# Optimization experiments

Hardware: AMD Instinct MI355X
Metric: run time of the kernel (lower is better)

Reference implementation:

```python
import jax, jax.numpy as jnp
from jax import lax
import numpy as np

H = 200           # mpnn_hidden_size
DEPTH = 3         # mpnn_depth
ATOM_FDIM = 39
BOND_FDIM = 11
B, NA, NB = 128, 48, 96   # molecules, atoms/mol, bonds/mol (padded fixed size)
L, VOCAB = 1000, 26       # protein length, amino-acid vocab
KERNALS = [3, 5, 7]
PROT_FILTERS = [50, 96, 128, 200]
FC_DIMS = [400, 200, 100, 1]


def setup_inputs() -> dict:
    key = jax.random.key(0)
    ks = jax.random.split(key, 32)
    s = 0.05
    inp = {}
    inp["fatoms"] = jax.random.normal(ks[0], (B, NA, ATOM_FDIM), jnp.float32)
    inp["fbonds"] = jax.random.normal(ks[1], (B, NB, ATOM_FDIM + BOND_FDIM), jnp.float32)
    inp["agraph"] = jax.random.randint(ks[2], (B, NA, 6), 0, NB)
    inp["bgraph"] = jax.random.randint(ks[3], (B, NB, 6), 0, NB)
    inp["protein_seq"] = jax.random.randint(ks[4], (B, L), 0, VOCAB)
    # MPNN weights (stored as (in, out) matrices; W_i and W_h have no bias)
    inp["W_i"] = jax.random.normal(ks[5], (ATOM_FDIM + BOND_FDIM, H), jnp.float32) * s
    inp["W_h"] = jax.random.normal(ks[6], (H, H), jnp.float32) * s
    inp["W_o_w"] = jax.random.normal(ks[7], (ATOM_FDIM + H, H), jnp.float32) * s
    inp["W_o_b"] = jax.random.normal(ks[8], (H,), jnp.float32) * s
    # protein embedding + CNN
    inp["embed_protein"] = jax.random.normal(ks[9], (VOCAB, PROT_FILTERS[0]), jnp.float32) * s
    for i, k in enumerate(KERNALS):
        inp[f"conv{i}_w"] = jax.random.normal(ks[10 + 2 * i], (PROT_FILTERS[i + 1], PROT_FILTERS[i], k), jnp.float32) * s
        inp[f"conv{i}_b"] = jax.random.normal(ks[11 + 2 * i], (PROT_FILTERS[i + 1],), jnp.float32) * s
    # CPI fc head 400 -> 200 -> 100 -> 1
    for i in range(3):
        inp[f"fc{i}_w"] = jax.random.normal(ks[16 + 2 * i], (FC_DIMS[i], FC_DIMS[i + 1]), jnp.float32) * s
        inp[f"fc{i}_b"] = jax.random.normal(ks[17 + 2 * i], (FC_DIMS[i + 1],), jnp.float32) * s
    return inp


def reference(fatoms, fbonds, agraph, bgraph, protein_seq,
              W_i, W_h, W_o_w, W_o_b, embed_protein,
              conv0_w, conv0_b, conv1_w, conv1_b, conv2_w, conv2_b,
              fc0_w, fc0_b, fc1_w, fc1_b, fc2_w, fc2_b):
    # ---- MPNN over all molecules (vmapped single_molecule_forward) ----
    def mol(fa, fb, ag, bg):
        binput = fb @ W_i                      # (NB, H)
        message = jax.nn.relu(binput)
        for _ in range(DEPTH - 1):
            nei = message[bg].sum(axis=1)      # gather (NB,6,H) -> sum -> (NB,H)
            message = jax.nn.relu(binput + nei @ W_h)
        nei = message[ag].sum(axis=1)          # (NA, H)
        atom_h = jax.nn.relu(jnp.concatenate([fa, nei], axis=1) @ W_o_w + W_o_b)
        return atom_h.mean(axis=0)             # (H,)

    embeddings = jax.vmap(mol)(fatoms, fbonds, agraph, bgraph)  # (B, H)

    # ---- protein CNN tower ----
    pv = embed_protein[protein_seq]            # (B, L, 50)
    pv = pv.transpose(0, 2, 1)                 # (B, 50, L)
    for w, b, k in ((conv0_w, conv0_b, KERNALS[0]),
                    (conv1_w, conv1_b, KERNALS[1]),
                    (conv2_w, conv2_b, KERNALS[2])):
        pv = lax.conv_general_dilated(pv, w, window_strides=(1,),
                                      padding=[(k // 2, k // 2)],
                                      dimension_numbers=("NCH", "OIH", "NCH"))
        pv = jax.nn.relu(pv + b[None, :, None])
    protein_vector = pv.max(axis=2)            # adaptive_max_pool1d(out=1) -> (B, 200)

    # ---- CPI fc head ----
    x = jnp.concatenate([embeddings, protein_vector], axis=1)  # (B, 400)
    x = jax.nn.relu(x @ fc0_w + fc0_b)
    x = jax.nn.relu(x @ fc1_w + fc1_b)
    x = x @ fc2_w + fc2_b
    return x                                   # (B, 1)
```

## Files before the change

kernel.cpp:

```cpp
#include <hip/hip_runtime.h>
#include <hip/hip_bf16.h>
#include <cstddef>

#define H 200
#define NA 48
#define NBB 96
#define BATCH 128
#define AFD 39
#define BFD 50
#define LP 1000
#define CATD (AFD + H)
#define APB 8
#define BIPB 16

typedef unsigned short ushort_t;
typedef __bf16 bf16x8 __attribute__((ext_vector_type(8)));
typedef float f32x16 __attribute__((ext_vector_type(16)));
typedef unsigned uint32x4 __attribute__((ext_vector_type(4)));

union U16B { uint4 u; bf16x8 b; };
static __device__ __forceinline__ bf16x8 as_bf16x8(uint4 u) { U16B x; x.u = u; return x.b; }
union U16B2 { uint32x4 u; bf16x8 b; };
static __device__ __forceinline__ bf16x8 as_bf16x8v(uint32x4 u) { U16B2 x; x.u = u; return x.b; }

static __device__ __forceinline__ ushort_t f2bf(float f) {
    union { float f; unsigned u; } a; a.f = f;
    unsigned r = (a.u + 0x7FFFu + ((a.u >> 16) & 1u)) >> 16;
    return (ushort_t)r;
}

static __device__ __forceinline__ uint32x4 gload16(const ushort_t* base, unsigned voff) {
    uint32x4 r;
    asm volatile("global_load_dwordx4 %0, %1, %2"
                 : "=&v"(r) : "v"(voff), "s"(base));
    return r;
}

template <int COUT, int CIN, int CP, int K>
static __device__ __forceinline__ void prep_one(int t, const float* __restrict__ w,
                                                ushort_t* __restrict__ Wb) {
    constexpr int NC = CP / 16;
    constexpr int NS = K * NC;
    int j = t & 7;
    int lane = (t >> 3) & 63;
    int s = (t >> 9) % NS;
    int ct = (t >> 9) / NS;
    int co = ct * 32 + (lane & 31);
    int tt = s / NC, cc = s % NC;
    int ci = cc * 16 + ((lane >> 5) & 1) * 8 + j;
    float v = 0.f;
    if (co < COUT && ci < CIN) v = w[((size_t)co * CIN + ci) * K + tt];
    Wb[t] = f2bf(v);
}

#define MNS 13
#define PREP_T0 (4 * 12 * 512)
#define PREP_T1 (PREP_T0 + 4 * 30 * 512)
#define PREP_T2 (PREP_T1 + 8 * 56 * 512)
#define PREP_T3 (PREP_T2 + 51200)
#define PREP_T4 (PREP_T3 + 8 * MNS * 512)

__global__ __launch_bounds__(256) void k_prep_all(
        const float* __restrict__ c0w, const float* __restrict__ c1w,
        const float* __restrict__ c2w, const float* __restrict__ Wh,
        float* __restrict__ x,
        ushort_t* __restrict__ Wb0, ushort_t* __restrict__ Wb1,
        ushort_t* __restrict__ Wb2, ushort_t* __restrict__ Wbh) {
    int tid = blockIdx.x * 256 + threadIdx.x;
    if (tid < PREP_T0) prep_one<96, 50, 64, 3>(tid, c0w, Wb0);
    else if (tid < PREP_T1) prep_one<128, 96, 96, 5>(tid - PREP_T0, c1w, Wb1);
    else if (tid < PREP_T2) prep_one<200, 128, 128, 7>(tid - PREP_T1, c2w, Wb2);
    else if (tid < PREP_T3) x[tid - PREP_T2] = 0.f;
    else if (tid < PREP_T4) {
        int t = tid - PREP_T3;
        int j = t & 7;
        int lane = (t >> 3) & 63;
        int s = (t >> 9) % MNS;
        int tile = (t >> 9) / MNS;
        int co = tile * 32 + (lane & 31);
        int ci = s * 16 + ((lane >> 5) & 1) * 8 + j;
        float v = 0.f;
        if (co < H && ci < H) v = Wh[ci * H + co];
        Wbh[t] = f2bf(v);
    }
}

template <int CP, int K, int COUT, int CO_WAVES, int L_WAVES, bool FMAX, bool EMB>
static __device__ __forceinline__ void conv_body(
        const ushort_t* __restrict__ act, const int* __restrict__ seq,
        const float* __restrict__ emb, const ushort_t* __restrict__ Wb,
        const float* __restrict__ bias, void* __restrict__ outv,
        ushort_t* __restrict__ Xs) {
    constexpr int NC = CP / 16;
    constexpr int NS = K * NC;
    constexpr int P = K / 2;
    constexpr int PITCH = CP + 8;
    constexpr int LTILE = 64 * L_WAVES;
    constexpr int ROWS = LTILE + K - 1;
    constexpr int CPR = CP / 8;
    constexpr int D = 4;

    int b = blockIdx.z, lb = blockIdx.x;
    int l0 = lb * LTILE;
    int tid = threadIdx.x;

    if (EMB) {
        const int* seqb = seq + (size_t)b * LP;
        for (int idx = tid; idx < ROWS * CPR; idx += 256) {
            int r = idx / CPR, c = idx % CPR;
            int l = l0 - P + r;
            uint4 v = {0u, 0u, 0u, 0u};
            if ((unsigned)l < (unsigned)LP) {
                int s = seqb[l];
                const float* e = emb + (size_t)s * 50;
                ushort_t h[8];
#pragma unroll
                for (int j = 0; j < 8; ++j) {
                    int cc = c * 8 + j;
                    h[j] = (cc < 50) ? f2bf(e[cc]) : (ushort_t)0;
                }
                v.x = (unsigned)h[0] | ((unsigned)h[1] << 16);
                v.y = (unsigned)h[2] | ((unsigned)h[3] << 16);
                v.z = (unsigned)h[4] | ((unsigned)h[5] << 16);
                v.w = (unsigned)h[6] | ((unsigned)h[7] << 16);
            }
            *(uint4*)(Xs + r * PITCH + c * 8) = v;
        }
    } else {
        const ushort_t* actb = act + (size_t)b * LP * CP;
        for (int idx = tid; idx < ROWS * CPR; idx += 256) {
            int r = idx / CPR, c = idx % CPR;
            int l = l0 - P + r;
            uint4 v = {0u, 0u, 0u, 0u};
            if ((unsigned)l < (unsigned)LP) v = *(const uint4*)(actb + (size_t)l * CP + c * 8);
            *(uint4*)(Xs + r * PITCH + c * 8) = v;
        }
    }

    int lane = tid & 63, wv = tid >> 6;
    int cw = wv % CO_WAVES, lw = wv / CO_WAVES;
    int ln31 = lane & 31, half = lane >> 5;

    unsigned abase0 = (unsigned)(cw * 2) * (unsigned)NS * 1024u + (unsigned)lane * 16u;
    unsigned abase1 = abase0 + (unsigned)NS * 1024u;
    int bbase = (lw * 64 + ln31) * PITCH + half * 8;

    f32x16 acc[2][2];
#pragma unroll
    for (int ct = 0; ct < 2; ++ct)
#pragma unroll
        for (int lt = 0; lt < 2; ++lt)
#pragma unroll
            for (int r = 0; r < 16; ++r) acc[ct][lt][r] = 0.f;

    __syncthreads();

    uint32x4 ra0[D], ra1[D];
#pragma unroll
    for (int d = 0; d < D; ++d) {
        ra0[d] = gload16(Wb, abase0 + (unsigned)(d * 1024));
        ra1[d] = gload16(Wb, abase1 + (unsigned)(d * 1024));
    }

    uint4 bC0 = *(const uint4*)(Xs + bbase);
    uint4 bC1 = *(const uint4*)(Xs + bbase + 32 * PITCH);

#pragma unroll
    for (int s = 0; s < NS; ++s) {
        int sn = (s + 1 < NS) ? s + 1 : NS - 1;
        int tn = sn / NC, ccn = sn % NC;
        int off = bbase + tn * PITCH + ccn * 16;
        uint4 bN0 = *(const uint4*)(Xs + off);
        uint4 bN1 = *(const uint4*)(Xs + off + 32 * PITCH);

        {
            const int rem = NS - 1 - s;
            const int allow = 2 * ((D - 1) < rem ? (D - 1) : rem);
            asm volatile("s_waitcnt vmcnt(%0)" :: "i"(allow) : "memory");
            __builtin_amdgcn_sched_barrier(0);
        }

        uint32x4 a0 = ra0[s % D];
        uint32x4 a1 = ra1[s % D];

        acc[0][0] = __builtin_amdgcn_mfma_f32_32x32x16_bf16(
            as_bf16x8v(a0), as_bf16x8(bC0), acc[0][0], 0, 0, 0);
        acc[1][0] = __builtin_amdgcn_mfma_f32_32x32x16_bf16(
            as_bf16x8v(a1), as_bf16x8(bC0), acc[1][0], 0, 0, 0);
        acc[0][1] = __builtin_amdgcn_mfma_f32_32x32x16_bf16(
            as_bf16x8v(a0), as_bf16x8(bC1), acc[0][1], 0, 0, 0);
        acc[1][1] = __builtin_amdgcn_mfma_f32_32x32x16_bf16(
            as_bf16x8v(a1), as_bf16x8(bC1), acc[1][1], 0, 0, 0);

        if (s + D < NS) {
            ra0[s % D] = gload16(Wb, abase0 + (unsigned)((s + D) * 1024));
            ra1[s % D] = gload16(Wb, abase1 + (unsigned)((s + D) * 1024));
        }

        bC0 = bN0; bC1 = bN1;
    }

    if (!FMAX) {
        ushort_t* out = (ushort_t*)outv + (size_t)b * LP * COUT;
#pragma unroll
        for (int ct = 0; ct < 2; ++ct) {
            int cbase = (cw * 2 + ct) * 32 + 4 * half;
#pragma unroll
            for (int g = 0; g < 4; ++g) {
                int co = cbase + 8 * g;
                if (co >= COUT) continue;
                float4 bv = *(const float4*)(bias + co);
#pragma unroll
                for (int lt = 0; lt < 2; ++lt) {
                    int l = l0 + lw * 64 + lt * 32 + ln31;
                    if (l < LP) {
                        ushort_t h0 = f2bf(fmaxf(acc[ct][lt][4 * g + 0] + bv.x, 0.f));
                        ushort_t h1 = f2bf(fmaxf(acc[ct][lt][4 * g + 1] + bv.y, 0.f));
                        ushort_t h2 = f2bf(fmaxf(acc[ct][lt][4 * g + 2] + bv.z, 0.f));
                        ushort_t h3 = f2bf(fmaxf(acc[ct][lt][4 * g + 3] + bv.w, 0.f));
                        uint2 o;
                        o.x = (unsigned)h0 | ((unsigned)h1 << 16);
                        o.y = (unsigned)h2 | ((unsigned)h3 << 16);
                        *(uint2*)(out + (size_t)l * COUT + co) = o;
                    }
                }
            }
        }
    } else {
        float* xout = (float*)outv;
#pragma unroll
        for (int ct = 0; ct < 2; ++ct) {
            float mx[16];
#pragma unroll
            for (int r = 0; r < 16; ++r) mx[r] = -3.0e38f;
#pragma unroll
            for (int lt = 0; lt < 2; ++lt) {
                int l = l0 + lw * 64 + lt * 32 + ln31;
                if (l < LP) {
#pragma unroll
                    for (int r = 0; r < 16; ++r) mx[r] = fmaxf(mx[r], acc[ct][lt][r]);
                }
            }
#pragma unroll
            for (int r = 0; r < 16; ++r) {
#pragma unroll
                for (int off = 1; off < 32; off <<= 1)
                    mx[r] = fmaxf(mx[r], __shfl_xor(mx[r], off, 64));
            }
            if (ln31 == 0) {
                int cbase = (cw * 2 + ct) * 32 + 4 * half;
#pragma unroll
                for (int r = 0; r < 16; ++r) {
                    int co = cbase + (r & 3) + 8 * (r >> 2);
                    if (co < COUT) {
                        float v = fmaxf(mx[r] + bias[co], 0.f);
                        atomicMax((int*)&xout[(size_t)b * 400 + 200 + co], __float_as_int(v));
                    }
                }
            }
        }
    }
}

__global__ __launch_bounds__(256, 3) void k_conv0(
        const int* __restrict__ seq, const float* __restrict__ emb,
        const ushort_t* __restrict__ Wb, const float* __restrict__ bias,
        ushort_t* __restrict__ out) {
    __shared__ __align__(16) ushort_t Xs[(128 + 2) * (64 + 8)];
    conv_body<64, 3, 96, 2, 2, false, true>(nullptr, seq, emb, Wb, bias, out, Xs);
}
__global__ __launch_bounds__(256, 3) void k_conv1(
        const ushort_t* __restrict__ act, const ushort_t* __restrict__ Wb,
        const float* __restrict__ bias, ushort_t* __restrict__ out) {
    __shared__ __align__(16) ushort_t Xs[(128 + 4) * (96 + 8)];
    conv_body<96, 5, 128, 2, 2, false, false>(act, nullptr, nullptr, Wb, bias, out, Xs);
}
__global__ __launch_bounds__(256, 3) void k_conv2(
        const ushort_t* __restrict__ act, const ushort_t* __restrict__ Wb,
        const float* __restrict__ bias, float* __restrict__ x) {
    __shared__ __align__(16) ushort_t Xs[(64 + 6) * (128 + 8)];
    conv_body<128, 7, 200, 4, 1, true, false>(act, nullptr, nullptr, Wb, bias, x, Xs);
}

__global__ __launch_bounds__(256) void k_bond_input(
        const float* __restrict__ fbonds, const float* __restrict__ Wi,
        float* __restrict__ binput, float* __restrict__ msg) {
    int bond0 = blockIdx.x * BIPB;
    __shared__ float fb[BIPB][BFD];
    int tid = threadIdx.x;
    for (int idx = tid; idx < BIPB * BFD; idx += 256)
        fb[idx / BFD][idx % BFD] = fbonds[(size_t)bond0 * BFD + idx];
    __syncthreads();
    if (tid < H) {
        float acc[BIPB];
#pragma unroll
        for (int q = 0; q < BIPB; ++q) acc[q] = 0.f;
#pragma unroll 5
        for (int k = 0; k < BFD; ++k) {
            float w = Wi[k * H + tid];
#pragma unroll
            for (int q = 0; q < BIPB; ++q) acc[q] += fb[q][k] * w;
        }
#pragma unroll
        for (int q = 0; q < BIPB; ++q) {
            size_t o = (size_t)(bond0 + q) * H + tid;
            binput[o] = acc[q];
            msg[o] = fmaxf(acc[q], 0.f);
        }
    }
}

#define MPITCH 216
__global__ __launch_bounds__(256) void k_msg_mfma(
        const float* __restrict__ msgIn, const float* __restrict__ binput,
        const int* __restrict__ bgraph, const ushort_t* __restrict__ Wbh,
        float* __restrict__ msgOut) {
    __shared__ __align__(16) ushort_t Xs[32 * MPITCH];
    __shared__ int idxs[32 * 6];
    constexpr int D = 4;
    int m0 = blockIdx.x * 32;
    int tid = threadIdx.x;

    if (tid < 192) {
        int r = tid / 6, j = tid - r * 6;
        int m = m0 + r;
        int mol = m / NBB;
        idxs[tid] = mol * NBB + bgraph[(size_t)m * 6 + j];
    }
    __syncthreads();

    for (int it = tid; it < 32 * 26; it += 256) {
        int r = it / 26, c = it - r * 26;
        uint4 v = {0u, 0u, 0u, 0u};
        if (c < 25) {
            float sv[8];
#pragma unroll
            for (int k = 0; k < 8; ++k) sv[k] = 0.f;
#pragma unroll
            for (int j = 0; j < 6; ++j) {
                const float* row = msgIn + (size_t)idxs[r * 6 + j] * H + c * 8;
                float4 a = *(const float4*)row;
                float4 b = *(const float4*)(row + 4);
                sv[0] += a.x; sv[1] += a.y; sv[2] += a.z; sv[3] += a.w;
                sv[4] += b.x; sv[5] += b.y; sv[6] += b.z; sv[7] += b.w;
            }
            v.x = (unsigned)f2bf(sv[0]) | ((unsigned)f2bf(sv[1]) << 16);
            v.y = (unsigned)f2bf(sv[2]) | ((unsigned)f2bf(sv[3]) << 16);
            v.z = (unsigned)f2bf(sv[4]) | ((unsigned)f2bf(sv[5]) << 16);
            v.w = (unsigned)f2bf(sv[6]) | ((unsigned)f2bf(sv[7]) << 16);
        }
        *(uint4*)(Xs + r * MPITCH + c * 8) = v;
    }

    int lane = tid & 63, wv = tid >> 6;
    int ln31 = lane & 31, half = lane >> 5;
    unsigned abase0 = (unsigned)(wv * 2) * (unsigned)MNS * 1024u + (unsigned)lane * 16u;
    unsigned abase1 = abase0 + (unsigned)MNS * 1024u;
    int bbase = ln31 * MPITCH + half * 8;

    f32x16 acc[2];
#pragma unroll
    for (int ct = 0; ct < 2; ++ct)
#pragma unroll
        for (int r = 0; r < 16; ++r) acc[ct][r] = 0.f;

    __syncthreads();

    uint32x4 ra0[D], ra1[D];
#pragma unroll
    for (int d = 0; d < D; ++d) {
        ra0[d] = gload16(Wbh, abase0 + (unsigned)(d * 1024));
        ra1[d] = gload16(Wbh, abase1 + (unsigned)(d * 1024));
    }

    uint4 bC = *(const uint4*)(Xs + bbase);

#pragma unroll
    for (int s = 0; s < MNS; ++s) {
        int sn = (s + 1 < MNS) ? s + 1 : MNS - 1;
        uint4 bN = *(const uint4*)(Xs + bbase + sn * 16);

        {
            const int rem = MNS - 1 - s;
            const int allow = 2 * ((D - 1) < rem ? (D - 1) : rem);
            asm volatile("s_waitcnt vmcnt(%0)" :: "i"(allow) : "memory");
            __builtin_amdgcn_sched_barrier(0);
        }

        uint32x4 a0 = ra0[s % D];
        uint32x4 a1 = ra1[s % D];
        acc[0] = __builtin_amdgcn_mfma_f32_32x32x16_bf16(
            as_bf16x8v(a0), as_bf16x8(bC), acc[0], 0, 0, 0);
        acc[1] = __builtin_amdgcn_mfma_f32_32x32x16_bf16(
            as_bf16x8v(a1), as_bf16x8(bC), acc[1], 0, 0, 0);

        if (s + D < MNS) {
            ra0[s % D] = gload16(Wbh, abase0 + (unsigned)((s + D) * 1024));
            ra1[s % D] = gload16(Wbh, abase1 + (unsigned)((s + D) * 1024));
        }
        bC = bN;
    }

    int m = m0 + ln31;
    const float* bi = binput + (size_t)m * H;
    float* outp = msgOut + (size_t)m * H;
#pragma unroll
    for (int ct = 0; ct < 2; ++ct) {
        int cbase = (wv * 2 + ct) * 32 + 4 * half;
#pragma unroll
        for (int g = 0; g < 4; ++g) {
            int co = cbase + 8 * g;
            if (co >= H) continue;
            float4 b4 = *(const float4*)(bi + co);
            float4 o;
            o.x = fmaxf(acc[ct][4 * g + 0] + b4.x, 0.f);
            o.y = fmaxf(acc[ct][4 * g + 1] + b4.y, 0.f);
            o.z = fmaxf(acc[ct][4 * g + 2] + b4.z, 0.f);
            o.w = fmaxf(acc[ct][4 * g + 3] + b4.w, 0.f);
            *(float4*)(outp + co) = o;
        }
    }
}

__global__ __launch_bounds__(256) void k_atom(
        const float* __restrict__ msg, const float* __restrict__ fatoms,
        const int* __restrict__ agraph, const float* __restrict__ Wo,
        const float* __restrict__ Wob, float* __restrict__ x) {
    const int grpPerMol = NA / APB;
    int b = blockIdx.x / grpPerMol;
    int grp = blockIdx.x % grpPerMol;
    int atom0 = grp * APB;
    __shared__ int idxs[APB * 6];
    __shared__ float cat[APB][CATD];
    int tid = threadIdx.x;
    if (tid < APB * 6) idxs[tid] = agraph[((size_t)(b * NA + atom0)) * 6 + tid];
    for (int idx = tid; idx < APB * AFD; idx += 256) {
        int q = idx / AFD, c = idx % AFD;
        cat[q][c] = fatoms[((size_t)(b * NA + atom0 + q)) * AFD + c];
    }
    __syncthreads();
    if (tid < H) {
        const float* base = msg + (size_t)b * NBB * H;
#pragma unroll
        for (int q = 0; q < APB; ++q) {
            float s = 0.f;
#pragma unroll
            for (int j = 0; j < 6; ++j) s += base[(size_t)idxs[q * 6 + j] * H + tid];
            cat[q][AFD + tid] = s;
        }
    }
    __syncthreads();
    if (tid < H) {
        float bb = Wob[tid];
        float acc[APB];
#pragma unroll
        for (int q = 0; q < APB; ++q) acc[q] = bb;
#pragma unroll 4
        for (int k = 0; k < CATD; ++k) {
            float w = Wo[k * H + tid];
#pragma unroll
            for (int q = 0; q < APB; ++q) acc[q] += cat[q][k] * w;
        }
        float s = 0.f;
#pragma unroll
        for (int q = 0; q < APB; ++q) s += fmaxf(acc[q], 0.f);
        atomicAdd(&x[(size_t)b * 400 + tid], s * (1.f / NA));
    }
}

__global__ __launch_bounds__(256) void k_fc(
        const float* __restrict__ x,
        const float* __restrict__ w0, const float* __restrict__ b0,
        const float* __restrict__ w1, const float* __restrict__ b1,
        const float* __restrict__ w2, const float* __restrict__ b2,
        float* __restrict__ out) {
    int b = blockIdx.x, tid = threadIdx.x;
    __shared__ float xr[400];
    __shared__ float h1[200];
    __shared__ float h2[100];
    for (int i = tid; i < 400; i += 256) xr[i] = x[(size_t)b * 400 + i];
    __syncthreads();
    if (tid < 200) {
        float a = b0[tid];
#pragma unroll 4
        for (int k = 0; k < 400; ++k) a += xr[k] * w0[k * 200 + tid];
        h1[tid] = fmaxf(a, 0.f);
    }
    __syncthreads();
    if (tid < 100) {
        float a = b1[tid];
#pragma unroll 4
        for (int k = 0; k < 200; ++k) a += h1[k] * w1[k * 100 + tid];
        h2[tid] = fmaxf(a, 0.f);
    }
    __syncthreads();
    if (tid == 0) {
        float a = b2[0];
#pragma unroll 4
        for (int k = 0; k < 100; ++k) a += h2[k] * w2[k];
        out[b] = a;
    }
}

extern "C" void kernel_launch(void* const* d_in, const int* in_sizes, int n_in,
                              void* d_out, int out_size, void* d_ws, size_t ws_size,
                              hipStream_t stream) {
    const float* fatoms = (const float*)d_in[0];
    const float* fbonds = (const float*)d_in[1];
    const int* agraph = (const int*)d_in[2];
    const int* bgraph = (const int*)d_in[3];
    const int* seq = (const int*)d_in[4];
    const float* Wi = (const float*)d_in[5];
    const float* Wh = (const float*)d_in[6];
    const float* Wo = (const float*)d_in[7];
    const float* Wob = (const float*)d_in[8];
    const float* embp = (const float*)d_in[9];
    const float* c0w = (const float*)d_in[10];
    const float* c0b = (const float*)d_in[11];
    const float* c1w = (const float*)d_in[12];
    const float* c1b = (const float*)d_in[13];
    const float* c2w = (const float*)d_in[14];
    const float* c2b = (const float*)d_in[15];
    const float* fc0w = (const float*)d_in[16];
    const float* fc0b = (const float*)d_in[17];
    const float* fc1w = (const float*)d_in[18];
    const float* fc1b = (const float*)d_in[19];
    const float* fc2w = (const float*)d_in[20];
    const float* fc2b = (const float*)d_in[21];

    float* ws = (float*)d_ws;
    float* binput = ws;
    float* msgA = binput + 2457600;
    float* msgB = msgA + 2457600;
    float* x = msgB + 2457600;
    ushort_t* u = (ushort_t*)(x + 51200);
    ushort_t* act1 = u;
    ushort_t* act2 = act1 + 12288000;
    ushort_t* Wb0 = act2 + 16384000;
    ushort_t* Wb1 = Wb0 + 24576;
    ushort_t* Wb2 = Wb1 + 61440;
    ushort_t* Wbh = Wb2 + 229376;

    k_prep_all<<<(PREP_T4 + 255) / 256, 256, 0, stream>>>(c0w, c1w, c2w, Wh, x,
                                                          Wb0, Wb1, Wb2, Wbh);

    k_bond_input<<<BATCH * NBB / BIPB, 256, 0, stream>>>(fbonds, Wi, binput, msgA);
    k_msg_mfma<<<BATCH * NBB / 32, 256, 0, stream>>>(msgA, binput, bgraph, Wbh, msgB);
    k_msg_mfma<<<BATCH * NBB / 32, 256, 0, stream>>>(msgB, binput, bgraph, Wbh, msgA);
    k_atom<<<BATCH * NA / APB, 256, 0, stream>>>(msgA, fatoms, agraph, Wo, Wob, x);

    k_conv0<<<dim3(8, 1, BATCH), 256, 0, stream>>>(seq, embp, Wb0, c0b, act1);
    k_conv1<<<dim3(8, 1, BATCH), 256, 0, stream>>>(act1, Wb1, c1b, act2);
    k_conv2<<<dim3(16, 1, BATCH), 256, 0, stream>>>(act2, Wb2, c2b, x);

    k_fc<<<BATCH, 256, 0, stream>>>(x, fc0w, fc0b, fc1w, fc1b, fc2w, fc2b, (float*)d_out);
}
```

Baseline: 345.2 us.

## Horizontally fuse independent MPNN and protein CNN kernels into shared launches

Merges the weight-prep and bond-input kernels into one launch. It also pairs each message-passing step, and then the atom readout, with a conv layer of the protein tower in a single grid, dispatching on blockIdx.x, so that 9 launches become 5. The MPNN and CNN branches are independent, so their blocks can run concurrently and fill the GPU better while paying fewer launch gaps. The cost is that shared-memory buffers are aliased between the branches and that the message kernel now inherits the conv kernels' (256,3) launch bounds. That can tighten its register budget and cause spills.

After: 331.0 us. -4.1%, faster.

```diff
diff --git a/kernel.cpp b/kernel.cpp
--- a/kernel.cpp
+++ b/kernel.cpp
@@ -59,14 +59,14 @@
 #define PREP_T2 (PREP_T1 + 8 * 56 * 512)
 #define PREP_T3 (PREP_T2 + 51200)
 #define PREP_T4 (PREP_T3 + 8 * MNS * 512)
-
-__global__ __launch_bounds__(256) void k_prep_all(
-        const float* __restrict__ c0w, const float* __restrict__ c1w,
+#define PREP_BLKS (PREP_T4 / 256)
+
+static __device__ __forceinline__ void prep_body(
+        int tid, const float* __restrict__ c0w, const float* __restrict__ c1w,
         const float* __restrict__ c2w, const float* __restrict__ Wh,
-        float* __restrict__ x,
-        ushort_t* __restrict__ Wb0, ushort_t* __restrict__ Wb1,
-        ushort_t* __restrict__ Wb2, ushort_t* __restrict__ Wbh) {
-    int tid = blockIdx.x * 256 + threadIdx.x;
+        float* __restrict__ x, ushort_t* __restrict__ Wb0,
+        ushort_t* __restrict__ Wb1, ushort_t* __restrict__ Wb2,
+        ushort_t* __restrict__ Wbh) {
     if (tid < PREP_T0) prep_one<96, 50, 64, 3>(tid, c0w, Wb0);
     else if (tid < PREP_T1) prep_one<128, 96, 96, 5>(tid - PREP_T0, c1w, Wb1);
     else if (tid < PREP_T2) prep_one<200, 128, 128, 7>(tid - PREP_T1, c2w, Wb2);
@@ -262,63 +262,13 @@
     }
 }
 
-__global__ __launch_bounds__(256, 3) void k_conv0(
-        const int* __restrict__ seq, const float* __restrict__ emb,
-        const ushort_t* __restrict__ Wb, const float* __restrict__ bias,
-        ushort_t* __restrict__ out) {
-    __shared__ __align__(16) ushort_t Xs[(128 + 2) * (64 + 8)];
-    conv_body<64, 3, 96, 2, 2, false, true>(nullptr, seq, emb, Wb, bias, out, Xs);
-}
-__global__ __launch_bounds__(256, 3) void k_conv1(
-        const ushort_t* __restrict__ act, const ushort_t* __restrict__ Wb,
-        const float* __restrict__ bias, ushort_t* __restrict__ out) {
-    __shared__ __align__(16) ushort_t Xs[(128 + 4) * (96 + 8)];
-    conv_body<96, 5, 128, 2, 2, false, false>(act, nullptr, nullptr, Wb, bias, out, Xs);
-}
-__global__ __launch_bounds__(256, 3) void k_conv2(
-        const ushort_t* __restrict__ act, const ushort_t* __restrict__ Wb,
-        const float* __restrict__ bias, float* __restrict__ x) {
-    __shared__ __align__(16) ushort_t Xs[(64 + 6) * (128 + 8)];
-    conv_body<128, 7, 200, 4, 1, true, false>(act, nullptr, nullptr, Wb, bias, x, Xs);
-}
-
-__global__ __launch_bounds__(256) void k_bond_input(
-        const float* __restrict__ fbonds, const float* __restrict__ Wi,
-        float* __restrict__ binput, float* __restrict__ msg) {
-    int bond0 = blockIdx.x * BIPB;
-    __shared__ float fb[BIPB][BFD];
-    int tid = threadIdx.x;
-    for (int idx = tid; idx < BIPB * BFD; idx += 256)
-        fb[idx / BFD][idx % BFD] = fbonds[(size_t)bond0 * BFD + idx];
-    __syncthreads();
-    if (tid < H) {
-        float acc[BIPB];
-#pragma unroll
-        for (int q = 0; q < BIPB; ++q) acc[q] = 0.f;
-#pragma unroll 5
-        for (int k = 0; k < BFD; ++k) {
-            float w = Wi[k * H + tid];
-#pragma unroll
-            for (int q = 0; q < BIPB; ++q) acc[q] += fb[q][k] * w;
-        }
-#pragma unroll
-        for (int q = 0; q < BIPB; ++q) {
-            size_t o = (size_t)(bond0 + q) * H + tid;
-            binput[o] = acc[q];
-            msg[o] = fmaxf(acc[q], 0.f);
-        }
-    }
-}
-
 #define MPITCH 216
-__global__ __launch_bounds__(256) void k_msg_mfma(
-        const float* __restrict__ msgIn, const float* __restrict__ binput,
+static __device__ __forceinline__ void msg_body(
+        int blk, const float* __restrict__ msgIn, const float* __restrict__ binput,
         const int* __restrict__ bgraph, const ushort_t* __restrict__ Wbh,
-        float* __restrict__ msgOut) {
-    __shared__ __align__(16) ushort_t Xs[32 * MPITCH];
-    __shared__ int idxs[32 * 6];
+        float* __restrict__ msgOut, ushort_t* __restrict__ Xs, int* __restrict__ idxs) {
     constexpr int D = 4;
-    int m0 = blockIdx.x * 32;
+    int m0 = blk * 32;
     int tid = threadIdx.x;
 
     if (tid < 192) {
@@ -366,7 +316,7 @@
 
     __syncthreads();
 
-    uint32x4 ra0[D], ra1[D];
+    uint32x4 ra0[4], ra1[4];
 #pragma unroll
     for (int d = 0; d < D; ++d) {
         ra0[d] = gload16(Wbh, abase0 + (unsigned)(d * 1024));
@@ -422,16 +372,42 @@
     }
 }
 
-__global__ __launch_bounds__(256) void k_atom(
-        const float* __restrict__ msg, const float* __restrict__ fatoms,
+static __device__ __forceinline__ void bond_body(
+        int blk, const float* __restrict__ fbonds, const float* __restrict__ Wi,
+        float* __restrict__ binput, float* __restrict__ msg, float (*fb)[BFD]) {
+    int bond0 = blk * BIPB;
+    int tid = threadIdx.x;
+    for (int idx = tid; idx < BIPB * BFD; idx += 256)
+        fb[idx / BFD][idx % BFD] = fbonds[(size_t)bond0 * BFD + idx];
+    __syncthreads();
+    if (tid < H) {
+        float acc[BIPB];
+#pragma unroll
+        for (int q = 0; q < BIPB; ++q) acc[q] = 0.f;
+#pragma unroll 5
+        for (int k = 0; k < BFD; ++k) {
+            float w = Wi[k * H + tid];
+#pragma unroll
+            for (int q = 0; q < BIPB; ++q) acc[q] += fb[q][k] * w;
+        }
+#pragma unroll
+        for (int q = 0; q < BIPB; ++q) {
+            size_t o = (size_t)(bond0 + q) * H + tid;
+            binput[o] = acc[q];
+            msg[o] = fmaxf(acc[q], 0.f);
+        }
+    }
+}
+
+static __device__ __forceinline__ void atom_body(
+        int blk, const float* __restrict__ msg, const float* __restrict__ fatoms,
         const int* __restrict__ agraph, const float* __restrict__ Wo,
-        const float* __restrict__ Wob, float* __restrict__ x) {
+        const float* __restrict__ Wob, float* __restrict__ x,
+        float (*cat)[CATD], int* __restrict__ idxs) {
     const int grpPerMol = NA / APB;
-    int b = blockIdx.x / grpPerMol;
-    int grp = blockIdx.x % grpPerMol;
+    int b = blk / grpPerMol;
+    int grp = blk % grpPerMol;
     int atom0 = grp * APB;
-    __shared__ int idxs[APB * 6];
-    __shared__ float cat[APB][CATD];
     int tid = threadIdx.x;
     if (tid < APB * 6) idxs[tid] = agraph[((size_t)(b * NA + atom0)) * 6 + tid];
     for (int idx = tid; idx < APB * AFD; idx += 256) {
@@ -465,6 +441,74 @@
 #pragma unroll
         for (int q = 0; q < APB; ++q) s += fmaxf(acc[q], 0.f);
         atomicAdd(&x[(size_t)b * 400 + tid], s * (1.f / NA));
+    }
+}
+
+
+__global__ __launch_bounds__(256) void k_l0_prep_bond(
+        const float* __restrict__ c0w, const float* __restrict__ c1w,
+        const float* __restrict__ c2w, const float* __restrict__ Wh,
+        float* __restrict__ x, ushort_t* __restrict__ Wb0,
+        ushort_t* __restrict__ Wb1, ushort_t* __restrict__ Wb2,
+        ushort_t* __restrict__ Wbh,
+        const float* __restrict__ fbonds, const float* __restrict__ Wi,
+        float* __restrict__ binput, float* __restrict__ msgA) {
+    __shared__ float fb[BIPB][BFD];
+    int bid = blockIdx.x;
+    if (bid < PREP_BLKS) {
+        prep_body(bid * 256 + threadIdx.x, c0w, c1w, c2w, Wh, x, Wb0, Wb1, Wb2, Wbh);
+    } else {
+        bond_body(bid - PREP_BLKS, fbonds, Wi, binput, msgA, fb);
+    }
+}
+
+__global__ __launch_bounds__(256, 3) void k_l1_conv0_msg(
+        const int* __restrict__ seq, const float* __restrict__ emb,
+        const ushort_t* __restrict__ Wb0, const float* __restrict__ c0b,
+        ushort_t* __restrict__ act1,
+        const float* __restrict__ msgIn, const float* __restrict__ binput,
+        const int* __restrict__ bgraph, const ushort_t* __restrict__ Wbh,
+        float* __restrict__ msgOut) {
+    __shared__ __align__(16) ushort_t Sbuf[(128 + 2) * (64 + 8)];
+    if (blockIdx.x < 8) {
+        conv_body<64, 3, 96, 2, 2, false, true>(nullptr, seq, emb, Wb0, c0b, act1, Sbuf);
+    } else {
+        int blk = (blockIdx.x - 8) * 128 + blockIdx.z;
+        msg_body(blk, msgIn, binput, bgraph, Wbh, msgOut, Sbuf,
+                 (int*)(Sbuf + 32 * MPITCH));
+    }
+}
+
+__global__ __launch_bounds__(256, 3) void k_l2_conv1_msg(
+        const ushort_t* __restrict__ act1, const ushort_t* __restrict__ Wb1,
+        const float* __restrict__ c1b, ushort_t* __restrict__ act2,
+        const float* __restrict__ msgIn, const float* __restrict__ binput,
+        const int* __restrict__ bgraph, const ushort_t* __restrict__ Wbh,
+        float* __restrict__ msgOut) {
+    __shared__ __align__(16) ushort_t Sbuf[(128 + 4) * (96 + 8)];
+    if (blockIdx.x < 8) {
+        conv_body<96, 5, 128, 2, 2, false, false>(act1, nullptr, nullptr, Wb1, c1b, act2, Sbuf);
+    } else {
+        int blk = (blockIdx.x - 8) * 128 + blockIdx.z;
+        msg_body(blk, msgIn, binput, bgraph, Wbh, msgOut, Sbuf,
+                 (int*)(Sbuf + 32 * MPITCH));
+    }
+}
+
+__global__ __launch_bounds__(256, 3) void k_l3_conv2_atom(
+        const ushort_t* __restrict__ act2, const ushort_t* __restrict__ Wb2,
+        const float* __restrict__ c2b, float* __restrict__ x,
+        const float* __restrict__ msg, const float* __restrict__ fatoms,
+        const int* __restrict__ agraph, const float* __restrict__ Wo,
+        const float* __restrict__ Wob) {
+    __shared__ __align__(16) ushort_t Sbuf[(64 + 6) * (128 + 8)];
+    if (blockIdx.x < 16) {
+        conv_body<128, 7, 200, 4, 1, true, false>(act2, nullptr, nullptr, Wb2, c2b, x, Sbuf);
+    } else {
+        int blk = (blockIdx.x - 16) * 128 + blockIdx.z;
+        float (*cat)[CATD] = (float (*)[CATD])Sbuf;
+        int* idxs = (int*)((char*)Sbuf + APB * CATD * 4);
+        atom_body(blk, msg, fatoms, agraph, Wo, Wob, x, cat, idxs);
     }
 }
 
@@ -541,17 +585,17 @@
     ushort_t* Wb2 = Wb1 + 61440;
     ushort_t* Wbh = Wb2 + 229376;
 
-    k_prep_all<<<(PREP_T4 + 255) / 256, 256, 0, stream>>>(c0w, c1w, c2w, Wh, x,
-                                                          Wb0, Wb1, Wb2, Wbh);
-
-    k_bond_input<<<BATCH * NBB / BIPB, 256, 0, stream>>>(fbonds, Wi, binput, msgA);
-    k_msg_mfma<<<BATCH * NBB / 32, 256, 0, stream>>>(msgA, binput, bgraph, Wbh, msgB);
-    k_msg_mfma<<<BATCH * NBB / 32, 256, 0, stream>>>(msgB, binput, bgraph, Wbh, msgA);
-    k_atom<<<BATCH * NA / APB, 256, 0, stream>>>(msgA, fatoms, agraph, Wo, Wob, x);
-
-    k_conv0<<<dim3(8, 1, BATCH), 256, 0, stream>>>(seq, embp, Wb0, c0b, act1);
-    k_conv1<<<dim3(8, 1, BATCH), 256, 0, stream>>>(act1, Wb1, c1b, act2);
-    k_conv2<<<dim3(16, 1, BATCH), 256, 0, stream>>>(act2, Wb2, c2b, x);
+    k_l0_prep_bond<<<PREP_BLKS + BATCH * NBB / BIPB, 256, 0, stream>>>(
+        c0w, c1w, c2w, Wh, x, Wb0, Wb1, Wb2, Wbh, fbonds, Wi, binput, msgA);
+
+    k_l1_conv0_msg<<<dim3(8 + 3, 1, BATCH), 256, 0, stream>>>(
+        seq, embp, Wb0, c0b, act1, msgA, binput, bgraph, Wbh, msgB);
+
+    k_l2_conv1_msg<<<dim3(8 + 3, 1, BATCH), 256, 0, stream>>>(
+        act1, Wb1, c1b, act2, msgB, binput, bgraph, Wbh, msgA);
+
+    k_l3_conv2_atom<<<dim3(16 + 6, 1, BATCH), 256, 0, stream>>>(
+        act2, Wb2, c2b, x, msgA, fatoms, agraph, Wo, Wob);
 
     k_fc<<<BATCH, 256, 0, stream>>>(x, fc0w, fc0b, fc1w, fc1b, fc2w, fc2b, (float*)d_out);
 }
```
